# Kernel optimization log

Measured on AMD Instinct MI355X. Metric: run time of the kernel, lower is better.

## Reference

```python
import jax, jax.numpy as jnp
import numpy as np

BLOCK_SIZE = 256


def setup_inputs() -> dict:
    key = jax.random.key(0)
    k1, k2, k3, k4 = jax.random.split(key, 4)
    B, T, C, H = 128, BLOCK_SIZE, 1024, 128
    x = jax.random.normal(k1, (B, T, C), dtype=jnp.float32)
    # nn.Linear(C, H, bias=False): y = x @ W^T with W (H, C); we store W^T as (C, H)
    scale = 1.0 / np.sqrt(C)
    Wq = jax.random.uniform(k2, (C, H), dtype=jnp.float32, minval=-scale, maxval=scale)
    Wk = jax.random.uniform(k3, (C, H), dtype=jnp.float32, minval=-scale, maxval=scale)
    Wv = jax.random.uniform(k4, (C, H), dtype=jnp.float32, minval=-scale, maxval=scale)
    return {"x": x, "Wq": Wq, "Wk": Wk, "Wv": Wv}


def reference(x, Wq, Wk, Wv):
    B, T, C = x.shape
    Q = jnp.einsum('btc,ch->bth', x, Wq)
    K = jnp.einsum('btc,ch->bth', x, Wk)
    V = jnp.einsum('btc,ch->bth', x, Wv)
    d_k = Q.shape[-1]
    scores = jnp.einsum('bth,bsh->bts', Q, K) / jnp.sqrt(jnp.asarray(d_k, x.dtype))
    causal = jnp.tril(jnp.ones((T, T), dtype=bool))  # tril buffer
    scores = jnp.where(causal, scores, -jnp.inf)
    S = jax.nn.softmax(scores, axis=-1)
    out = jnp.einsum('bts,bsh->bth', S, V)
    return out
```

## Files before the change

### kernel.cpp

```cpp
#include <hip/hip_runtime.h>

typedef float  f32x4  __attribute__((ext_vector_type(4)));
typedef short  s16x8  __attribute__((ext_vector_type(8)));
typedef short  s16x4  __attribute__((ext_vector_type(4)));

__device__ __forceinline__ unsigned short f2bf(float f) {
    unsigned int u = __float_as_uint(f);
    return (unsigned short)((u + 0x7FFFu + ((u >> 16) & 1u)) >> 16);
}

__device__ __forceinline__ s16x8 cvt8(f32x4 a, f32x4 b) {
    union { unsigned int u[4]; s16x8 v; } r;
    asm("v_cvt_pk_bf16_f32 %0, %1, %2" : "=v"(r.u[0]) : "v"(a[0]), "v"(a[1]));
    asm("v_cvt_pk_bf16_f32 %0, %1, %2" : "=v"(r.u[1]) : "v"(a[2]), "v"(a[3]));
    asm("v_cvt_pk_bf16_f32 %0, %1, %2" : "=v"(r.u[2]) : "v"(b[0]), "v"(b[1]));
    asm("v_cvt_pk_bf16_f32 %0, %1, %2" : "=v"(r.u[3]) : "v"(b[2]), "v"(b[3]));
    return r.v;
}

__device__ __forceinline__ void lds_barrier() {
    asm volatile("s_waitcnt lgkmcnt(0)" ::: "memory");
    __builtin_amdgcn_s_barrier();
    asm volatile("" ::: "memory");
}

__global__ void prep_wt(const float* __restrict__ Wq,
                        const float* __restrict__ Wk,
                        const float* __restrict__ Wv,
                        unsigned char* __restrict__ wt3) {
    int n = blockIdx.x;
    const float* W = (n < 128) ? Wq : ((n < 256) ? Wk : Wv);
    int h = n & 127;
    int n16 = n >> 4, lmn = n & 15;
    for (int k = threadIdx.x; k < 1024; k += blockDim.x) {
        unsigned short v = f2bf(W[(size_t)k * 128 + h]);
        int ks = k >> 6, rem = k & 63;
        int kkk = rem >> 5, l4_ = (rem >> 3) & 3, j = rem & 7;
        int lane = l4_ * 16 + lmn;
        size_t off = (size_t)(n16 * 32 + ks * 2 + kkk) * 1024 + lane * 16 + j * 2;
        *(unsigned short*)(wt3 + off) = v;
    }
}

__global__ __launch_bounds__(512, 4) void qkv_gemm(
    const float* __restrict__ x,
    const unsigned char* __restrict__ wt3,
    unsigned short* __restrict__ qo,
    unsigned short* __restrict__ ko,
    unsigned short* __restrict__ vto) {

    __shared__ char smem[16384];

    const int tid = threadIdx.x;
    const int bm  = blockIdx.x;
    const int lane = tid & 63, wid = tid >> 6;
    const int lm = lane & 15, l4 = lane >> 4;

    f32x4 acc[4][3];
#pragma unroll
    for (int i = 0; i < 4; ++i)
#pragma unroll
        for (int j = 0; j < 3; ++j) acc[i][j] = (f32x4)0.f;

    const int ar  = tid >> 3;
    const int ac8 = tid & 7;
    const float* xp = x + (size_t)(bm * 64 + ar) * 1024 + ac8 * 8;
    const int aw = ar * 128 + ((ac8 << 4) ^ ((ar & 7) << 4));

    const unsigned char* wb = wt3 + (size_t)lane * 16;
    int bqo[3];
#pragma unroll
    for (int ni = 0; ni < 3; ++ni) bqo[ni] = (wid * 3 + ni) * 32768;

    int arow[4];
#pragma unroll
    for (int mi = 0; mi < 4; ++mi) arow[mi] = mi * 16 + lm;

    f32x4 pa0 = *(const f32x4*)(xp);
    f32x4 pa1 = *(const f32x4*)(xp + 4);
    s16x8 bq[6];
#pragma unroll
    for (int ni = 0; ni < 3; ++ni) {
        bq[ni * 2]     = *(const s16x8*)(wb + bqo[ni]);
        bq[ni * 2 + 1] = *(const s16x8*)(wb + bqo[ni] + 1024);
    }
    *(s16x8*)(smem + aw) = cvt8(pa0, pa1);
    pa0 = *(const f32x4*)(xp + 64);
    pa1 = *(const f32x4*)(xp + 68);
    lds_barrier();

    for (int t = 0; t < 16; ++t) {
        const int ab = (t & 1) * 8192;
        {
            s16x8 af[4];
#pragma unroll
            for (int mi = 0; mi < 4; ++mi)
                af[mi] = *(const s16x8*)(smem + ab + arow[mi] * 128 +
                           ((l4 * 16) ^ ((arow[mi] & 7) << 4)));
            __builtin_amdgcn_s_setprio(1);
#pragma unroll
            for (int ni = 0; ni < 3; ++ni)
#pragma unroll
                for (int mi = 0; mi < 4; ++mi)
                    acc[mi][ni] = __builtin_amdgcn_mfma_f32_16x16x32_bf16(
                        af[mi], bq[ni * 2], acc[mi][ni], 0, 0, 0);
            __builtin_amdgcn_s_setprio(0);
        }
        {
            s16x8 af[4];
#pragma unroll
            for (int mi = 0; mi < 4; ++mi)
                af[mi] = *(const s16x8*)(smem + ab + arow[mi] * 128 +
                           ((64 + l4 * 16) ^ ((arow[mi] & 7) << 4)));
            __builtin_amdgcn_s_setprio(1);
#pragma unroll
            for (int ni = 0; ni < 3; ++ni)
#pragma unroll
                for (int mi = 0; mi < 4; ++mi)
                    acc[mi][ni] = __builtin_amdgcn_mfma_f32_16x16x32_bf16(
                        af[mi], bq[ni * 2 + 1], acc[mi][ni], 0, 0, 0);
            __builtin_amdgcn_s_setprio(0);
        }
        if (t < 15) {
            const unsigned char* wn = wb + (t + 1) * 2048;
#pragma unroll
            for (int ni = 0; ni < 3; ++ni) {
                bq[ni * 2]     = *(const s16x8*)(wn + bqo[ni]);
                bq[ni * 2 + 1] = *(const s16x8*)(wn + bqo[ni] + 1024);
            }
            *(s16x8*)(smem + (ab ^ 8192) + aw) = cvt8(pa0, pa1);
            if (t < 14) {
                pa0 = *(const f32x4*)(xp + (t + 2) * 64);
                pa1 = *(const f32x4*)(xp + (t + 2) * 64 + 4);
            }
            lds_barrier();
        }
    }

#pragma unroll
    for (int mi = 0; mi < 4; ++mi) {
        int m0 = bm * 64 + mi * 16 + l4 * 4;
#pragma unroll
        for (int ni = 0; ni < 3; ++ni) {
            int nb  = wid * 48 + ni * 16;
            int mat = nb >> 7;
            int col = (nb & 127) + lm;
            if (mat == 2) {
                int bb2 = m0 >> 8, tt = m0 & 255;
                s16x4 w4;
#pragma unroll
                for (int j = 0; j < 4; ++j) w4[j] = (short)f2bf(acc[mi][ni][j]);
                *(s16x4*)(vto + ((size_t)bb2 * 128 + col) * 256 + tt) = w4;
            } else {
                unsigned short* dst = (mat == 0) ? qo : ko;
#pragma unroll
                for (int j = 0; j < 4; ++j)
                    dst[(size_t)(m0 + j) * 128 + col] = f2bf(acc[mi][ni][j]);
            }
        }
    }
}

__global__ __launch_bounds__(512) void attn(
    const unsigned short* __restrict__ q,
    const unsigned short* __restrict__ k,
    const unsigned short* __restrict__ vt,
    float* __restrict__ out) {

    __shared__ char pbuf[65536];

    const int tid = threadIdx.x, wid = tid >> 6, lane = tid & 63;
    const int lm = lane & 15, l4 = lane >> 4;
    const int b = blockIdx.x >> 1, qt = blockIdx.x & 1;
    const int qbase = qt << 7;
    const int t0 = qbase + wid * 16;
    const int nfrags = (qbase + 128) >> 4;
    const int nkf    = (qbase + 128) >> 5;

    const unsigned short* qrow = q + (size_t)(b * 256 + t0 + lm) * 128 + l4 * 8;
    s16x8 qf[4];
#pragma unroll
    for (int kf = 0; kf < 4; ++kf) qf[kf] = *(const s16x8*)(qrow + kf * 32);

    f32x4 sacc[16];
#pragma unroll
    for (int i = 0; i < 16; ++i) sacc[i] = (f32x4)0.f;

    const unsigned short* kbase = k + (size_t)(b * 256) * 128 + l4 * 8;
#pragma unroll
    for (int nf = 0; nf < 16; ++nf) {
        if (nf < nfrags) {
#pragma unroll
            for (int kf = 0; kf < 4; ++kf) {
                s16x8 a = *(const s16x8*)(kbase + (size_t)(nf * 16 + lm) * 128 + kf * 32);
                sacc[nf] = __builtin_amdgcn_mfma_f32_16x16x32_bf16(a, qf[kf], sacc[nf], 0, 0, 0);
            }
        }
    }

    const float scale = 0.08838834764831845f;
    const int tg = t0 + lm;
    float mx = -1e30f;
#pragma unroll
    for (int nf = 0; nf < 16; ++nf) {
        if (nf < nfrags) {
#pragma unroll
            for (int j = 0; j < 4; ++j) {
                int kv = nf * 16 + l4 * 4 + j;
                float s = sacc[nf][j] * scale;
                s = (kv > tg) ? -1e30f : s;
                sacc[nf][j] = s;
                mx = fmaxf(mx, s);
            }
        }
    }
    mx = fmaxf(mx, __shfl_xor(mx, 16));
    mx = fmaxf(mx, __shfl_xor(mx, 32));
    float sum = 0.f;
#pragma unroll
    for (int nf = 0; nf < 16; ++nf) {
        if (nf < nfrags) {
#pragma unroll
            for (int j = 0; j < 4; ++j) {
                float p = __expf(sacc[nf][j] - mx);
                sacc[nf][j] = p;
                sum += p;
            }
        }
    }
    sum += __shfl_xor(sum, 16);
    sum += __shfl_xor(sum, 32);
    float rinv = 1.0f / sum;

    char* pw = pbuf + wid * 8192 + lm * 512;
#pragma unroll
    for (int nf = 0; nf < 16; ++nf) {
        if (nf < nfrags) {
            s16x4 w;
#pragma unroll
            for (int j = 0; j < 4; ++j) w[j] = (short)f2bf(sacc[nf][j] * rinv);
            *(s16x4*)(pw + ((nf * 32 + l4 * 8) ^ ((lm & 7) << 4))) = w;
        }
    }
    asm volatile("s_waitcnt lgkmcnt(0)" ::: "memory");

    f32x4 oacc[8];
#pragma unroll
    for (int i = 0; i < 8; ++i) oacc[i] = (f32x4)0.f;

    const unsigned short* vbase = vt + (size_t)b * 32768 + l4 * 8;
#pragma unroll
    for (int kvf = 0; kvf < 8; ++kvf) {
        if (kvf < nkf) {
            s16x8 pf = *(const s16x8*)(pbuf + wid * 8192 + lm * 512 +
                        ((kvf * 64 + l4 * 16) ^ ((lm & 7) << 4)));
#pragma unroll
            for (int hf = 0; hf < 8; ++hf) {
                s16x8 a = *(const s16x8*)(vbase + (size_t)(hf * 16 + lm) * 256 + kvf * 32);
                oacc[hf] = __builtin_amdgcn_mfma_f32_16x16x32_bf16(a, pf, oacc[hf], 0, 0, 0);
            }
        }
    }

    float* ob = out + (size_t)(b * 256 + t0 + lm) * 128 + l4 * 4;
#pragma unroll
    for (int hf = 0; hf < 8; ++hf)
        *(f32x4*)(ob + hf * 16) = oacc[hf];
}

extern "C" void kernel_launch(void* const* d_in, const int* in_sizes, int n_in,
                              void* d_out, int out_size, void* d_ws, size_t ws_size,
                              hipStream_t stream) {
    const float* x  = (const float*)d_in[0];
    const float* Wq = (const float*)d_in[1];
    const float* Wk = (const float*)d_in[2];
    const float* Wv = (const float*)d_in[3];
    float* out = (float*)d_out;

    char* ws = (char*)d_ws;
    unsigned char*  wt = (unsigned char*)(ws);
    unsigned short* qb = (unsigned short*)(ws + 786432);
    unsigned short* kb = (unsigned short*)(ws + 786432 + 8388608);
    unsigned short* vb = (unsigned short*)(ws + 786432 + 2 * 8388608);

    prep_wt<<<384, 256, 0, stream>>>(Wq, Wk, Wv, wt);
    qkv_gemm<<<512, 512, 0, stream>>>(x, wt, qb, kb, vb);
    attn<<<256, 512, 0, stream>>>(qb, kb, vb, out);
}
```

Baseline: 78.16 us.

## Double QKV GEMM M-tile to 128 rows with explicit double-buffered K loop

The QKV projection block now covers 128 rows of x instead of 64. Each weight fragment loaded from global memory therefore feeds twice as many MFMAs, which halves weight traffic per output and halves the grid to 256 blocks. The K loop is unrolled by two with separate even and odd weight register sets and two LDS buffers, so loads for the next step overlap compute on the current one. The cost is higher register and LDS use (occupancy hint lowered to 2) and fewer blocks than the MI355X has CUs, which may leave compute units idle.

```diff
diff --git a/kernel.cpp b/kernel.cpp
--- a/kernel.cpp
+++ b/kernel.cpp
@@ -42,104 +42,138 @@
     }
 }
 
-__global__ __launch_bounds__(512, 4) void qkv_gemm(
+__global__ __launch_bounds__(512, 2) void qkv_gemm(
     const float* __restrict__ x,
     const unsigned char* __restrict__ wt3,
     unsigned short* __restrict__ qo,
     unsigned short* __restrict__ ko,
     unsigned short* __restrict__ vto) {
 
-    __shared__ char smem[16384];
+    __shared__ char smem[32768];
 
     const int tid = threadIdx.x;
     const int bm  = blockIdx.x;
     const int lane = tid & 63, wid = tid >> 6;
     const int lm = lane & 15, l4 = lane >> 4;
 
-    f32x4 acc[4][3];
-#pragma unroll
-    for (int i = 0; i < 4; ++i)
+    f32x4 acc[8][3];
+#pragma unroll
+    for (int i = 0; i < 8; ++i)
 #pragma unroll
         for (int j = 0; j < 3; ++j) acc[i][j] = (f32x4)0.f;
 
-    const int ar  = tid >> 3;
-    const int ac8 = tid & 7;
-    const float* xp = x + (size_t)(bm * 64 + ar) * 1024 + ac8 * 8;
-    const int aw = ar * 128 + ((ac8 << 4) ^ ((ar & 7) << 4));
+    const int ar  = tid >> 2;
+    const int acb = (tid & 3) * 16;
+    const float* xp = x + (size_t)(bm * 128 + ar) * 1024 + acb;
+    const int aswz = (ar & 7) << 4;
+    const int aw0 = ar * 128 + ((acb * 2) ^ aswz);
+    const int aw1 = ar * 128 + ((acb * 2 + 16) ^ aswz);
 
     const unsigned char* wb = wt3 + (size_t)lane * 16;
-    int bqo[3];
-#pragma unroll
-    for (int ni = 0; ni < 3; ++ni) bqo[ni] = (wid * 3 + ni) * 32768;
-
-    int arow[4];
-#pragma unroll
-    for (int mi = 0; mi < 4; ++mi) arow[mi] = mi * 16 + lm;
-
-    f32x4 pa0 = *(const f32x4*)(xp);
-    f32x4 pa1 = *(const f32x4*)(xp + 4);
-    s16x8 bq[6];
-#pragma unroll
-    for (int ni = 0; ni < 3; ++ni) {
-        bq[ni * 2]     = *(const s16x8*)(wb + bqo[ni]);
-        bq[ni * 2 + 1] = *(const s16x8*)(wb + bqo[ni] + 1024);
-    }
-    *(s16x8*)(smem + aw) = cvt8(pa0, pa1);
-    pa0 = *(const f32x4*)(xp + 64);
-    pa1 = *(const f32x4*)(xp + 68);
-    lds_barrier();
-
-    for (int t = 0; t < 16; ++t) {
-        const int ab = (t & 1) * 8192;
-        {
-            s16x8 af[4];
-#pragma unroll
-            for (int mi = 0; mi < 4; ++mi)
-                af[mi] = *(const s16x8*)(smem + ab + arow[mi] * 128 +
-                           ((l4 * 16) ^ ((arow[mi] & 7) << 4)));
-            __builtin_amdgcn_s_setprio(1);
+    const unsigned char* wbq[3];
+#pragma unroll
+    for (int ni = 0; ni < 3; ++ni) wbq[ni] = wb + (size_t)(wid * 3 + ni) * 32768;
+
+    int arow[8];
+#pragma unroll
+    for (int mi = 0; mi < 8; ++mi) arow[mi] = mi * 16 + lm;
+
+    s16x8 af[8];
+    s16x8 bqE0[3], bqE1[3], bqO0[3], bqO1[3];
+    f32x4 pa0, pa1, pa2, pa3;
+
+#define AFREAD(AB, KOFF)                                                       \
+    do {                                                                       \
+        _Pragma("unroll")                                                      \
+        for (int mi = 0; mi < 8; ++mi)                                         \
+            af[mi] = *(const s16x8*)(smem + (AB) + arow[mi] * 128 +            \
+                      (((KOFF) + l4 * 16) ^ ((arow[mi] & 7) << 4)));           \
+    } while (0)
+
+#define MFMA3(BQ)                                                              \
+    do {                                                                       \
+        __builtin_amdgcn_s_setprio(1);                                         \
+        _Pragma("unroll")                                                      \
+        for (int ni = 0; ni < 3; ++ni)                                         \
+            _Pragma("unroll")                                                  \
+            for (int mi = 0; mi < 8; ++mi)                                     \
+                acc[mi][ni] = __builtin_amdgcn_mfma_f32_16x16x32_bf16(         \
+                    af[mi], (BQ)[ni], acc[mi][ni], 0, 0, 0);                   \
+        __builtin_amdgcn_s_setprio(0);                                         \
+    } while (0)
+
+    {
+        f32x4 a0 = *(const f32x4*)(xp);
+        f32x4 a1 = *(const f32x4*)(xp + 4);
+        f32x4 a2 = *(const f32x4*)(xp + 8);
+        f32x4 a3 = *(const f32x4*)(xp + 12);
+#pragma unroll
+        for (int ni = 0; ni < 3; ++ni) {
+            bqE0[ni] = *(const s16x8*)(wbq[ni]);
+            bqE1[ni] = *(const s16x8*)(wbq[ni] + 1024);
+        }
+        *(s16x8*)(smem + aw0) = cvt8(a0, a1);
+        *(s16x8*)(smem + aw1) = cvt8(a2, a3);
+        pa0 = *(const f32x4*)(xp + 64);
+        pa1 = *(const f32x4*)(xp + 68);
+        pa2 = *(const f32x4*)(xp + 72);
+        pa3 = *(const f32x4*)(xp + 76);
+        lds_barrier();
+    }
+
+    for (int tp = 0; tp < 8; ++tp) {
+        const int t = tp * 2;
+        AFREAD(0, 0);
+        MFMA3(bqE0);
+#pragma unroll
+        for (int ni = 0; ni < 3; ++ni)
+            bqO0[ni] = *(const s16x8*)(wbq[ni] + (t + 1) * 2048);
+        AFREAD(0, 64);
+        MFMA3(bqE1);
+#pragma unroll
+        for (int ni = 0; ni < 3; ++ni)
+            bqO1[ni] = *(const s16x8*)(wbq[ni] + (t + 1) * 2048 + 1024);
+        *(s16x8*)(smem + 16384 + aw0) = cvt8(pa0, pa1);
+        *(s16x8*)(smem + 16384 + aw1) = cvt8(pa2, pa3);
+        if (tp < 7) {
+            const float* xq = xp + (t + 2) * 64;
+            pa0 = *(const f32x4*)(xq);
+            pa1 = *(const f32x4*)(xq + 4);
+            pa2 = *(const f32x4*)(xq + 8);
+            pa3 = *(const f32x4*)(xq + 12);
+        }
+        lds_barrier();
+
+        AFREAD(16384, 0);
+        MFMA3(bqO0);
+        if (tp < 7) {
 #pragma unroll
             for (int ni = 0; ni < 3; ++ni)
-#pragma unroll
-                for (int mi = 0; mi < 4; ++mi)
-                    acc[mi][ni] = __builtin_amdgcn_mfma_f32_16x16x32_bf16(
-                        af[mi], bq[ni * 2], acc[mi][ni], 0, 0, 0);
-            __builtin_amdgcn_s_setprio(0);
-        }
-        {
-            s16x8 af[4];
-#pragma unroll
-            for (int mi = 0; mi < 4; ++mi)
-                af[mi] = *(const s16x8*)(smem + ab + arow[mi] * 128 +
-                           ((64 + l4 * 16) ^ ((arow[mi] & 7) << 4)));
-            __builtin_amdgcn_s_setprio(1);
+                bqE0[ni] = *(const s16x8*)(wbq[ni] + (t + 2) * 2048);
+        }
+        AFREAD(16384, 64);
+        MFMA3(bqO1);
+        if (tp < 7) {
 #pragma unroll
             for (int ni = 0; ni < 3; ++ni)
-#pragma unroll
-                for (int mi = 0; mi < 4; ++mi)
-                    acc[mi][ni] = __builtin_amdgcn_mfma_f32_16x16x32_bf16(
-                        af[mi], bq[ni * 2 + 1], acc[mi][ni], 0, 0, 0);
-            __builtin_amdgcn_s_setprio(0);
-        }
-        if (t < 15) {
-            const unsigned char* wn = wb + (t + 1) * 2048;
-#pragma unroll
-            for (int ni = 0; ni < 3; ++ni) {
-                bq[ni * 2]     = *(const s16x8*)(wn + bqo[ni]);
-                bq[ni * 2 + 1] = *(const s16x8*)(wn + bqo[ni] + 1024);
-            }
-            *(s16x8*)(smem + (ab ^ 8192) + aw) = cvt8(pa0, pa1);
-            if (t < 14) {
-                pa0 = *(const f32x4*)(xp + (t + 2) * 64);
-                pa1 = *(const f32x4*)(xp + (t + 2) * 64 + 4);
-            }
+                bqE1[ni] = *(const s16x8*)(wbq[ni] + (t + 2) * 2048 + 1024);
+            *(s16x8*)(smem + aw0) = cvt8(pa0, pa1);
+            *(s16x8*)(smem + aw1) = cvt8(pa2, pa3);
+            const float* xq = xp + (t + 3) * 64;
+            pa0 = *(const f32x4*)(xq);
+            pa1 = *(const f32x4*)(xq + 4);
+            pa2 = *(const f32x4*)(xq + 8);
+            pa3 = *(const f32x4*)(xq + 12);
             lds_barrier();
         }
     }
 
-#pragma unroll
-    for (int mi = 0; mi < 4; ++mi) {
-        int m0 = bm * 64 + mi * 16 + l4 * 4;
+#undef AFREAD
+#undef MFMA3
+
+#pragma unroll
+    for (int mi = 0; mi < 8; ++mi) {
+        int m0 = bm * 128 + mi * 16 + l4 * 4;
 #pragma unroll
         for (int ni = 0; ni < 3; ++ni) {
             int nb  = wid * 48 + ni * 16;
@@ -284,6 +318,6 @@
     unsigned short* vb = (unsigned short*)(ws + 786432 + 2 * 8388608);
 
     prep_wt<<<384, 256, 0, stream>>>(Wq, Wk, Wv, wt);
-    qkv_gemm<<<512, 512, 0, stream>>>(x, wt, qb, kb, vb);
+    qkv_gemm<<<256, 512, 0, stream>>>(x, wt, qb, kb, vb);
     attn<<<256, 512, 0, stream>>>(qb, kb, vb, out);
 }
```

Result: no change. 76.85 us (-1.7%).

## Double GEMM row tile to 128 with 1024-thread blocks and deeper B prefetch

Applied to the files above, without the earlier changes.

The QKV projection GEMM now uses 1024-thread blocks that each cover 128 rows of x. Two groups of 8 waves split the rows, and each wave group shares the same weight columns. The K loop is unrolled by two, with separate even and odd B register sets, so weight fragments are loaded one half-step ahead of the MFMAs that use them, and LDS reads are interleaved with MFMA groups. This halves the grid to 256 blocks and doubles the LDS A tile. The aim is to give more in-flight memory per block and better latency hiding, at the cost of more registers per block, possibly lower occupancy, and fewer blocks than CUs.

```diff
diff --git a/kernel.cpp b/kernel.cpp
--- a/kernel.cpp
+++ b/kernel.cpp
@@ -42,19 +42,21 @@
     }
 }
 
-__global__ __launch_bounds__(512, 4) void qkv_gemm(
+__global__ __launch_bounds__(1024, 4) void qkv_gemm(
     const float* __restrict__ x,
     const unsigned char* __restrict__ wt3,
     unsigned short* __restrict__ qo,
     unsigned short* __restrict__ ko,
     unsigned short* __restrict__ vto) {
 
-    __shared__ char smem[16384];
+    __shared__ char smem[32768];
 
     const int tid = threadIdx.x;
     const int bm  = blockIdx.x;
     const int lane = tid & 63, wid = tid >> 6;
     const int lm = lane & 15, l4 = lane >> 4;
+    const int wn = wid & 7;
+    const int wm = wid >> 3;
 
     f32x4 acc[4][3];
 #pragma unroll
@@ -64,85 +66,100 @@
 
     const int ar  = tid >> 3;
     const int ac8 = tid & 7;
-    const float* xp = x + (size_t)(bm * 64 + ar) * 1024 + ac8 * 8;
+    const float* xp = x + (size_t)(bm * 128 + ar) * 1024 + ac8 * 8;
     const int aw = ar * 128 + ((ac8 << 4) ^ ((ar & 7) << 4));
 
-    const unsigned char* wb = wt3 + (size_t)lane * 16;
-    int bqo[3];
-#pragma unroll
-    for (int ni = 0; ni < 3; ++ni) bqo[ni] = (wid * 3 + ni) * 32768;
+    const unsigned char* wb = wt3 + (size_t)(wn * 3) * 32768 + (size_t)lane * 16;
 
     int arow[4];
 #pragma unroll
-    for (int mi = 0; mi < 4; ++mi) arow[mi] = mi * 16 + lm;
-
-    f32x4 pa0 = *(const f32x4*)(xp);
-    f32x4 pa1 = *(const f32x4*)(xp + 4);
-    s16x8 bq[6];
-#pragma unroll
-    for (int ni = 0; ni < 3; ++ni) {
-        bq[ni * 2]     = *(const s16x8*)(wb + bqo[ni]);
-        bq[ni * 2 + 1] = *(const s16x8*)(wb + bqo[ni] + 1024);
-    }
-    *(s16x8*)(smem + aw) = cvt8(pa0, pa1);
-    pa0 = *(const f32x4*)(xp + 64);
-    pa1 = *(const f32x4*)(xp + 68);
-    lds_barrier();
-
-    for (int t = 0; t < 16; ++t) {
-        const int ab = (t & 1) * 8192;
-        {
-            s16x8 af[4];
-#pragma unroll
-            for (int mi = 0; mi < 4; ++mi)
-                af[mi] = *(const s16x8*)(smem + ab + arow[mi] * 128 +
-                           ((l4 * 16) ^ ((arow[mi] & 7) << 4)));
-            __builtin_amdgcn_s_setprio(1);
-#pragma unroll
-            for (int ni = 0; ni < 3; ++ni)
-#pragma unroll
-                for (int mi = 0; mi < 4; ++mi)
-                    acc[mi][ni] = __builtin_amdgcn_mfma_f32_16x16x32_bf16(
-                        af[mi], bq[ni * 2], acc[mi][ni], 0, 0, 0);
-            __builtin_amdgcn_s_setprio(0);
-        }
-        {
-            s16x8 af[4];
-#pragma unroll
-            for (int mi = 0; mi < 4; ++mi)
-                af[mi] = *(const s16x8*)(smem + ab + arow[mi] * 128 +
-                           ((64 + l4 * 16) ^ ((arow[mi] & 7) << 4)));
-            __builtin_amdgcn_s_setprio(1);
-#pragma unroll
-            for (int ni = 0; ni < 3; ++ni)
-#pragma unroll
-                for (int mi = 0; mi < 4; ++mi)
-                    acc[mi][ni] = __builtin_amdgcn_mfma_f32_16x16x32_bf16(
-                        af[mi], bq[ni * 2 + 1], acc[mi][ni], 0, 0, 0);
-            __builtin_amdgcn_s_setprio(0);
-        }
-        if (t < 15) {
-            const unsigned char* wn = wb + (t + 1) * 2048;
-#pragma unroll
-            for (int ni = 0; ni < 3; ++ni) {
-                bq[ni * 2]     = *(const s16x8*)(wn + bqo[ni]);
-                bq[ni * 2 + 1] = *(const s16x8*)(wn + bqo[ni] + 1024);
-            }
-            *(s16x8*)(smem + (ab ^ 8192) + aw) = cvt8(pa0, pa1);
-            if (t < 14) {
-                pa0 = *(const f32x4*)(xp + (t + 2) * 64);
-                pa1 = *(const f32x4*)(xp + (t + 2) * 64 + 4);
-            }
+    for (int mi = 0; mi < 4; ++mi) arow[mi] = wm * 64 + mi * 16 + lm;
+
+    s16x8 bqE0[3], bqE1[3], bqO0[3], bqO1[3];
+    f32x4 pa0, pa1;
+
+#define MFMA_HALF(AB, KOFF, BQ)                                                \
+    do {                                                                       \
+        s16x8 af0 = *(const s16x8*)(smem + (AB) + arow[0] * 128 +              \
+                     (((KOFF) + l4 * 16) ^ ((arow[0] & 7) << 4)));             \
+        s16x8 af1 = *(const s16x8*)(smem + (AB) + arow[1] * 128 +              \
+                     (((KOFF) + l4 * 16) ^ ((arow[1] & 7) << 4)));             \
+        _Pragma("unroll")                                                      \
+        for (int ni = 0; ni < 3; ++ni) {                                       \
+            acc[0][ni] = __builtin_amdgcn_mfma_f32_16x16x32_bf16(              \
+                af0, (BQ)[ni], acc[0][ni], 0, 0, 0);                           \
+            acc[1][ni] = __builtin_amdgcn_mfma_f32_16x16x32_bf16(              \
+                af1, (BQ)[ni], acc[1][ni], 0, 0, 0);                           \
+        }                                                                      \
+        s16x8 af2 = *(const s16x8*)(smem + (AB) + arow[2] * 128 +              \
+                     (((KOFF) + l4 * 16) ^ ((arow[2] & 7) << 4)));             \
+        s16x8 af3 = *(const s16x8*)(smem + (AB) + arow[3] * 128 +              \
+                     (((KOFF) + l4 * 16) ^ ((arow[3] & 7) << 4)));             \
+        _Pragma("unroll")                                                      \
+        for (int ni = 0; ni < 3; ++ni) {                                       \
+            acc[2][ni] = __builtin_amdgcn_mfma_f32_16x16x32_bf16(              \
+                af2, (BQ)[ni], acc[2][ni], 0, 0, 0);                           \
+            acc[3][ni] = __builtin_amdgcn_mfma_f32_16x16x32_bf16(              \
+                af3, (BQ)[ni], acc[3][ni], 0, 0, 0);                           \
+        }                                                                      \
+    } while (0)
+
+#define BLOAD(DST, T, KKK)                                                     \
+    do {                                                                       \
+        _Pragma("unroll")                                                      \
+        for (int ni = 0; ni < 3; ++ni)                                         \
+            (DST)[ni] = *(const s16x8*)(wb + ni * 32768 + (T) * 2048 +         \
+                                        (KKK) * 1024);                         \
+    } while (0)
+
+    {
+        f32x4 a0 = *(const f32x4*)(xp);
+        f32x4 a1 = *(const f32x4*)(xp + 4);
+        BLOAD(bqE0, 0, 0);
+        *(s16x8*)(smem + aw) = cvt8(a0, a1);
+        pa0 = *(const f32x4*)(xp + 64);
+        pa1 = *(const f32x4*)(xp + 68);
+        lds_barrier();
+    }
+
+    for (int tp = 0; tp < 8; ++tp) {
+        const int t = tp * 2;
+        BLOAD(bqE1, t, 1);
+        MFMA_HALF(0, 0, bqE0);
+        BLOAD(bqO0, t + 1, 0);
+        MFMA_HALF(0, 64, bqE1);
+        *(s16x8*)(smem + 16384 + aw) = cvt8(pa0, pa1);
+        if (tp < 7 || true) {
+            const float* xq = xp + (t + 2) * 64;
+            if (t + 2 < 16) {
+                pa0 = *(const f32x4*)(xq);
+                pa1 = *(const f32x4*)(xq + 4);
+            }
+        }
+        lds_barrier();
+
+        BLOAD(bqO1, t + 1, 1);
+        MFMA_HALF(16384, 0, bqO0);
+        if (tp < 7) BLOAD(bqE0, t + 2, 0);
+        MFMA_HALF(16384, 64, bqO1);
+        if (tp < 7) {
+            *(s16x8*)(smem + aw) = cvt8(pa0, pa1);
+            const float* xq = xp + (t + 3) * 64;
+            pa0 = *(const f32x4*)(xq);
+            pa1 = *(const f32x4*)(xq + 4);
             lds_barrier();
         }
     }
 
+#undef MFMA_HALF
+#undef BLOAD
+
 #pragma unroll
     for (int mi = 0; mi < 4; ++mi) {
-        int m0 = bm * 64 + mi * 16 + l4 * 4;
+        int m0 = bm * 128 + wm * 64 + mi * 16 + l4 * 4;
 #pragma unroll
         for (int ni = 0; ni < 3; ++ni) {
-            int nb  = wid * 48 + ni * 16;
+            int nb  = wn * 48 + ni * 16;
             int mat = nb >> 7;
             int col = (nb & 127) + lm;
             if (mat == 2) {
@@ -284,6 +301,6 @@
     unsigned short* vb = (unsigned short*)(ws + 786432 + 2 * 8388608);
 
     prep_wt<<<384, 256, 0, stream>>>(Wq, Wk, Wv, wt);
-    qkv_gemm<<<512, 512, 0, stream>>>(x, wt, qb, kb, vb);
+    qkv_gemm<<<256, 1024, 0, stream>>>(x, wt, qb, kb, vb);
     attn<<<256, 512, 0, stream>>>(qb, kb, vb, out);
 }
```

Measured after the change: 81.12 us. 3.8% more time.
